# Kernel tuning notes

Measured on AMD Instinct MI355X. Metric: run time of the kernel, lower is better.

## Reference

```python
import jax, jax.numpy as jnp
import numpy as np

N_NODES = 10000
N_EDGES = 320000
N_GSO = 2
BATCH = 4
F0, F1, F2 = 64, 128, 128
K = 3


def _spmm(rows, cols, vals, x_nbf):
    """Sparse GSO multiply: (S x) for x in node-major layout [N, B, F]."""
    src = x_nbf[cols] * vals[:, None, None]            # [E, B, F]
    return jax.ops.segment_sum(src, rows, num_segments=x_nbf.shape[0])


def _graph_filter(x, edge_index, edge_vals, W, b):
    """y = sum_e sum_k S_e^k x W[e,k] + b.
    x: [B, N, Fin]; edge_index: [E_gso, 2, nnz] int; edge_vals: [E_gso, nnz];
    W: [E_gso, K, Fin, Fout]; b: [Fout]."""
    z0 = x.transpose(1, 0, 2)                          # [N, B, Fin]
    n_gso, k_taps = W.shape[0], W.shape[1]
    out = jnp.zeros((z0.shape[0], z0.shape[1], W.shape[-1]), dtype=x.dtype)
    for e in range(n_gso):
        rows, cols = edge_index[e, 0], edge_index[e, 1]
        zk = z0                                        # tap k=0 is identity
        out = out + jnp.einsum('nbf,fg->nbg', zk, W[e, 0])
        for k in range(1, k_taps):
            zk = _spmm(rows, cols, edge_vals[e], zk)   # zk = S_e zk
            out = out + jnp.einsum('nbf,fg->nbg', zk, W[e, k])
    out = out + b
    return out.transpose(1, 0, 2)                      # [B, N, Fout]


def setup_inputs() -> dict:
    key = jax.random.key(0)
    ks = jax.random.split(key, 8)
    x = jax.random.normal(ks[0], (BATCH, N_NODES, F0), dtype=jnp.float32)
    edge_index = jax.random.randint(ks[1], (N_GSO, 2, N_EDGES), 0, N_NODES, dtype=jnp.int32)
    # scale edge values ~ 1/avg_degree to keep repeated diffusion stable
    edge_vals = jax.random.uniform(ks[2], (N_GSO, N_EDGES), dtype=jnp.float32) * (1.0 / 32.0)
    W1 = jax.random.normal(ks[3], (N_GSO, K, F0, F1), dtype=jnp.float32) * 0.05
    b1 = jax.random.normal(ks[4], (F1,), dtype=jnp.float32) * 0.05
    W2 = jax.random.normal(ks[5], (N_GSO, K, F1, F2), dtype=jnp.float32) * 0.05
    b2 = jax.random.normal(ks[6], (F2,), dtype=jnp.float32) * 0.05
    return {"x": x, "edge_index": edge_index, "edge_vals": edge_vals,
            "W1": W1, "b1": b1, "W2": W2, "b2": b2}


def reference(x, edge_index, edge_vals, W1, b1, W2, b2):
    h = _graph_filter(x, edge_index, edge_vals, W1, b1)
    h = _graph_filter(h, edge_index, edge_vals, W2, b2)
    return h[:, 0, :]                                  # idxTrainMovie = 0 -> [B, F2]
```

## Files before the change

kernel.cpp:

```cpp
#include <hip/hip_runtime.h>

#define N_NODES 10000
#define N_EDGES 320000
#define BCAP    96
#define NCPY    8

__device__ __forceinline__ unsigned short f2bf(float x) {
    unsigned int u = __float_as_uint(x);
    unsigned int r = (u + 0x7fff + ((u >> 16) & 1)) >> 16;
    return (unsigned short)r;
}
__device__ __forceinline__ float bfhi(unsigned int u) { return __uint_as_float(u & 0xffff0000u); }

__global__ void bucket_kernel(const int* __restrict__ ei, const float* __restrict__ ev,
                              int* __restrict__ cnt, unsigned int* __restrict__ bkt,
                              float* __restrict__ wA) {
    int j = blockIdx.x * 256 + threadIdx.x;
    int e = j / N_EDGES, t = j - e * N_EDGES;
    int r = ei[e * 2 * N_EDGES + t];
    int c = ei[e * 2 * N_EDGES + N_EDGES + t];
    float v = ev[e * N_EDGES + t];
    int pos = atomicAdd(&cnt[e * N_NODES + c], 1);
    if (pos < BCAP)
        bkt[(e * N_NODES + c) * BCAP + pos] = ((unsigned int)f2bf(v) << 16) | (unsigned int)r;
    if (r == 0)
        atomicAdd(&wA[c * 4 + (e ? 2 : 0)], v);
}

__global__ __launch_bounds__(256) void gstage1_kernel(
        const unsigned int* __restrict__ bkt, const int* __restrict__ cnt,
        float* __restrict__ wA) {
    int t = threadIdx.x;
    int gu = (blockIdx.x << 4) + (t >> 4);
    int li = t & 15;
    int e = (gu >= N_NODES) ? 1 : 0;
    int c = gu - e * N_NODES;
    int nc = cnt[e * N_NODES + c]; if (nc > BCAP) nc = BCAP;
    const unsigned int* bp = bkt + (e * N_NODES + c) * BCAP;
    int koff = e ? 2 : 0;
    float acc = 0.f;
    for (int p = li; p < nc; p += 16) {
        unsigned int u = bp[p];
        acc += bfhi(u) * wA[(u & 0xffff) * 4 + koff];
    }
    acc += __shfl_xor(acc, 1); acc += __shfl_xor(acc, 2);
    acc += __shfl_xor(acc, 4); acc += __shfl_xor(acc, 8);
    if (li == 0) wA[c * 4 + koff + 1] = acc;
}

__global__ __launch_bounds__(256) void gstage2_kernel(
        const unsigned int* __restrict__ bkt, const int* __restrict__ cnt,
        const float* __restrict__ wA, float4* __restrict__ wB0, float4* __restrict__ wB1) {
    int t = threadIdx.x;
    int gu = (blockIdx.x << 4) + (t >> 4);
    int li = t & 15;
    int e = (gu >= N_NODES) ? 1 : 0;
    int c = gu - e * N_NODES;
    int nc = cnt[e * N_NODES + c]; if (nc > BCAP) nc = BCAP;
    const unsigned int* bp = bkt + (e * N_NODES + c) * BCAP;
    const float4* wAp = (const float4*)wA;
    float x0 = 0.f, x1 = 0.f, x2 = 0.f;
    for (int p = li; p < nc; p += 16) {
        unsigned int u = bp[p];
        float v = bfhi(u);
        float4 wr = wAp[u & 0xffff];
        if (e == 0) { x0 += wr.y * v; x1 += wr.z * v; x2 += wr.w * v; }
        else        { x0 += wr.w * v; x1 += wr.x * v; x2 += wr.y * v; }
    }
    x0 += __shfl_xor(x0, 1); x0 += __shfl_xor(x0, 2); x0 += __shfl_xor(x0, 4); x0 += __shfl_xor(x0, 8);
    x1 += __shfl_xor(x1, 1); x1 += __shfl_xor(x1, 2); x1 += __shfl_xor(x1, 4); x1 += __shfl_xor(x1, 8);
    x2 += __shfl_xor(x2, 1); x2 += __shfl_xor(x2, 2); x2 += __shfl_xor(x2, 4); x2 += __shfl_xor(x2, 8);
    if (li == 0) {
        float4 o = make_float4(x0, x1, x2, 0.f);
        if (e == 0) wB0[c] = o; else wB1[c] = o;
    }
}

__global__ __launch_bounds__(256) void gstage3_kernel(
        const unsigned int* __restrict__ bkt, const int* __restrict__ cnt,
        const float4* __restrict__ wB0, const float4* __restrict__ wB1,
        float4* __restrict__ wC0, float4* __restrict__ wC1) {
    int t = threadIdx.x;
    int gu = (blockIdx.x << 4) + (t >> 4);
    int li = t & 15;
    int e = (gu >= N_NODES) ? 1 : 0;
    int c = gu - e * N_NODES;
    int nc = cnt[e * N_NODES + c]; if (nc > BCAP) nc = BCAP;
    const unsigned int* bp = bkt + (e * N_NODES + c) * BCAP;
    const float4* win = e ? wB1 : wB0;
    float x0 = 0.f, x1 = 0.f, x2 = 0.f;
    for (int p = li; p < nc; p += 16) {
        unsigned int u = bp[p];
        float v = bfhi(u);
        float4 wr = win[u & 0xffff];
        x0 += wr.x * v; x1 += wr.y * v; x2 += wr.z * v;
    }
    x0 += __shfl_xor(x0, 1); x0 += __shfl_xor(x0, 2); x0 += __shfl_xor(x0, 4); x0 += __shfl_xor(x0, 8);
    x1 += __shfl_xor(x1, 1); x1 += __shfl_xor(x1, 2); x1 += __shfl_xor(x1, 4); x1 += __shfl_xor(x1, 8);
    x2 += __shfl_xor(x2, 1); x2 += __shfl_xor(x2, 2); x2 += __shfl_xor(x2, 4); x2 += __shfl_xor(x2, 8);
    if (li == 0) {
        float4 o = make_float4(x0, x1, x2, 0.f);
        if (e == 0) wC0[c] = o; else wC1[c] = o;
    }
}

__global__ __launch_bounds__(256) void ugemm_kernel(const float* __restrict__ x,
                                                    const float* __restrict__ wA,
                                                    const float4* __restrict__ wB0,
                                                    const float4* __restrict__ wB1,
                                                    const float4* __restrict__ wC0,
                                                    const float4* __restrict__ wC1,
                                                    float* __restrict__ U8,
                                                    float* __restrict__ S8) {
    int t = threadIdx.x;
    int b = t >> 6, f = t & 63;
    int n0 = blockIdx.x * 16;
    int cp = blockIdx.x & (NCPY - 1);
    const float* xp = x + b * (N_NODES * 64) + f;
    const float4* wAp = (const float4*)wA;
    float acc[16];
    #pragma unroll
    for (int k = 0; k < 16; ++k) acc[k] = 0.f;
    float s0 = 0.f, s1 = 0.f, s2 = 0.f, s3 = 0.f;
    #pragma unroll
    for (int j = 0; j < 16; ++j) {
        int n = n0 + j;
        float4 a  = wAp[n];
        float4 p0 = wB0[n], p1 = wB1[n];
        float4 q0 = wC0[n], q1 = wC1[n];
        float xv = xp[n * 64];
        acc[0]  += a.x * xv;  acc[1]  += a.y * xv;
        acc[2]  += a.z * xv;  acc[3]  += a.w * xv;
        acc[4]  += p0.x * xv; acc[5]  += p0.y * xv; acc[6]  += p0.z * xv;
        acc[7]  += p1.x * xv; acc[8]  += p1.y * xv; acc[9]  += p1.z * xv;
        acc[10] += q0.x * xv; acc[11] += q0.y * xv; acc[12] += q0.z * xv;
        acc[13] += q1.x * xv; acc[14] += q1.y * xv; acc[15] += q1.z * xv;
        if (t == 0) { s0 += a.x; s1 += a.y; s2 += a.z; s3 += a.w; }
    }
    float* up = U8 + cp * 4096;
    #pragma unroll
    for (int k = 0; k < 16; ++k)
        atomicAdd(&up[k * 256 + t], acc[k]);
    if (t == 0) {
        float* sp = S8 + cp * 4;
        atomicAdd(&sp[0], s0); atomicAdd(&sp[1], s1);
        atomicAdd(&sp[2], s2); atomicAdd(&sp[3], s3);
    }
}

__global__ __launch_bounds__(512) void final_T_kernel(
        const float* __restrict__ x, const float* __restrict__ U8,
        const float* __restrict__ S8,
        const float* __restrict__ W1, const float* __restrict__ b1,
        float* __restrict__ T, float* __restrict__ out) {
    __shared__ float Ws[8192];
    __shared__ float src[256];
    int blk = blockIdx.x;
    int s = blk / 5, g = blk - s * 5;
    int t = threadIdx.x;
    if (blk == 0) out[t] = 0.f;
    const int w1off[5] = { 0, 8192, 16384, 32768, 40960 };
    const float4* wsrc = (const float4*)(W1 + w1off[s]);
    const float4* wsrc0 = (const float4*)(W1 + 24576);
    float4* wdst = (float4*)Ws;
    #pragma unroll
    for (int i = 0; i < 4; ++i) {
        float4 v = wsrc[i * 512 + t];
        if (s == 0) {
            float4 v2 = wsrc0[i * 512 + t];
            v.x += v2.x; v.y += v2.y; v.z += v2.z; v.w += v2.w;
        }
        wdst[i * 512 + t] = v;
    }
    if (t < 256) {
        const int hmap[5] = { -1, 0, 1, 2, 3 };
        const int umap[4][5] = {
            { 0, 1, 4,  8, 14 },
            { 1, 4, 10, 9, 15 },
            { 2, 5, 11, 3,  7 },
            { 3, 6, 12, 7, 13 },
        };
        int k = (g == 0) ? hmap[s] : umap[g - 1][s];
        float sv;
        if (k < 0) {
            sv = x[(t >> 6) * (N_NODES * 64) + (t & 63)];
        } else {
            sv = 0.f;
            #pragma unroll
            for (int c = 0; c < NCPY; ++c) sv += U8[c * 4096 + k * 256 + t];
        }
        src[t] = sv;
    }
    __syncthreads();
    int b = t >> 7, f1 = t & 127;
    const float* sp = src + b * 64;
    float acc = 0.f;
    #pragma unroll 16
    for (int f0 = 0; f0 < 64; ++f0)
        acc += sp[f0] * Ws[f0 * 128 + f1];
    if (s == 0) {
        if (g == 0) acc += b1[f1];
        else {
            float Sg = 0.f;
            #pragma unroll
            for (int c = 0; c < NCPY; ++c) Sg += S8[c * 4 + (g - 1)];
            acc += Sg * b1[f1];
        }
    }
    atomicAdd(&T[g * 512 + t], acc);
}

__global__ __launch_bounds__(512) void final_out_kernel(
        const float* __restrict__ T, const float* __restrict__ W2,
        const float* __restrict__ b2, float* __restrict__ out) {
    __shared__ float Ws[16384];
    __shared__ float Ts[512];
    int g = blockIdx.x;
    int t = threadIdx.x;
    const int w2off[5] = { 0, 16384, 32768, 65536, 81920 };
    const float4* wsrc = (const float4*)(W2 + w2off[g]);
    const float4* wsrc0 = (const float4*)(W2 + 49152);
    float4* wdst = (float4*)Ws;
    #pragma unroll
    for (int i = 0; i < 8; ++i) {
        float4 v = wsrc[i * 512 + t];
        if (g == 0) {
            float4 v2 = wsrc0[i * 512 + t];
            v.x += v2.x; v.y += v2.y; v.z += v2.z; v.w += v2.w;
        }
        wdst[i * 512 + t] = v;
    }
    Ts[t] = T[g * 512 + t];
    __syncthreads();
    int b = t >> 7, f2 = t & 127;
    const float* tp = Ts + b * 128;
    float acc = (g == 0) ? b2[f2] : 0.f;
    #pragma unroll 16
    for (int f1 = 0; f1 < 128; ++f1)
        acc += tp[f1] * Ws[f1 * 128 + f2];
    atomicAdd(&out[t], acc);
}

extern "C" void kernel_launch(void* const* d_in, const int* in_sizes, int n_in,
                              void* d_out, int out_size, void* d_ws, size_t ws_size,
                              hipStream_t stream) {
    const float* x  = (const float*)d_in[0];
    const int*   ei = (const int*)d_in[1];
    const float* ev = (const float*)d_in[2];
    const float* W1 = (const float*)d_in[3];
    const float* b1 = (const float*)d_in[4];
    const float* W2 = (const float*)d_in[5];
    const float* b2 = (const float*)d_in[6];
    float* out = (float*)d_out;

    char* ws = (char*)d_ws;
    size_t off = 0;
    auto alloc = [&](size_t bytes) { size_t o = off; off += (bytes + 255) & ~(size_t)255; return o; };
    size_t o_bkt   = alloc((size_t)2 * N_NODES * BCAP * 4);
    size_t o_zero  = off;
    size_t o_cnt   = alloc((size_t)2 * N_NODES * 4);
    size_t o_wA    = alloc((size_t)N_NODES * 4 * 4);
    size_t o_wB0   = alloc((size_t)N_NODES * 4 * 4);
    size_t o_wB1   = alloc((size_t)N_NODES * 4 * 4);
    size_t o_wC0   = alloc((size_t)N_NODES * 4 * 4);
    size_t o_wC1   = alloc((size_t)N_NODES * 4 * 4);
    size_t o_U     = alloc((size_t)NCPY * 16 * 256 * 4);
    size_t o_S     = alloc((size_t)NCPY * 4 * 4);
    size_t o_T     = alloc((size_t)5 * 512 * 4);
    size_t zero_bytes = off - o_zero;

    unsigned int* bkt = (unsigned int*)(ws + o_bkt);
    int*    cnt   = (int*)(ws + o_cnt);
    float*  wA    = (float*)(ws + o_wA);
    float4* wB0   = (float4*)(ws + o_wB0);
    float4* wB1   = (float4*)(ws + o_wB1);
    float4* wC0   = (float4*)(ws + o_wC0);
    float4* wC1   = (float4*)(ws + o_wC1);
    float*  U8    = (float*)(ws + o_U);
    float*  S8    = (float*)(ws + o_S);
    float*  T     = (float*)(ws + o_T);

    hipMemsetAsync(ws + o_zero, 0, zero_bytes, stream);

    bucket_kernel  <<<2500, 256, 0, stream>>>(ei, ev, cnt, bkt, wA);
    gstage1_kernel <<<1250, 256, 0, stream>>>(bkt, cnt, wA);
    gstage2_kernel <<<1250, 256, 0, stream>>>(bkt, cnt, wA, wB0, wB1);
    gstage3_kernel <<<1250, 256, 0, stream>>>(bkt, cnt, wB0, wB1, wC0, wC1);
    ugemm_kernel   <<<625,  256, 0, stream>>>(x, wA, wB0, wB1, wC0, wC1, U8, S8);
    final_T_kernel <<<25,   512, 0, stream>>>(x, U8, S8, W1, b1, T, out);
    final_out_kernel<<<5,   512, 0, stream>>>(T, W2, b2, out);
}
```

Measured before the change: 163.7 us.

## Replace global-atomic edge bucketing with histogram, scan, and shared-memory fill

Edge bucketing by column used to do one global atomicAdd per edge on a counter array. It now runs in three passes. Per-chunk, per-partition histograms are built in shared memory, an exclusive scan over chunks gives each block its base offsets, and a fill pass places edges using shared-memory atomics. This removes contention on global atomics but adds two kernel launches, a histogram workspace, and reads the edge arrays eight times, once per column partition.

```diff
diff --git a/kernel.cpp b/kernel.cpp
--- a/kernel.cpp
+++ b/kernel.cpp
@@ -4,6 +4,8 @@
 #define N_EDGES 320000
 #define BCAP    96
 #define NCPY    8
+#define NCH     64
+#define HSTRIDE 1280
 
 __device__ __forceinline__ unsigned short f2bf(float x) {
     unsigned int u = __float_as_uint(x);
@@ -12,19 +14,74 @@
 }
 __device__ __forceinline__ float bfhi(unsigned int u) { return __uint_as_float(u & 0xffff0000u); }
 
-__global__ void bucket_kernel(const int* __restrict__ ei, const float* __restrict__ ev,
-                              int* __restrict__ cnt, unsigned int* __restrict__ bkt,
-                              float* __restrict__ wA) {
-    int j = blockIdx.x * 256 + threadIdx.x;
-    int e = j / N_EDGES, t = j - e * N_EDGES;
-    int r = ei[e * 2 * N_EDGES + t];
-    int c = ei[e * 2 * N_EDGES + N_EDGES + t];
-    float v = ev[e * N_EDGES + t];
-    int pos = atomicAdd(&cnt[e * N_NODES + c], 1);
-    if (pos < BCAP)
-        bkt[(e * N_NODES + c) * BCAP + pos] = ((unsigned int)f2bf(v) << 16) | (unsigned int)r;
-    if (r == 0)
-        atomicAdd(&wA[c * 4 + (e ? 2 : 0)], v);
+__global__ __launch_bounds__(256) void hist_kernel(
+        const int* __restrict__ ei, int* __restrict__ hist) {
+    __shared__ int h[1250];
+    int bid = blockIdx.x;
+    int p = bid & 7;
+    int ec = bid >> 3;
+    int e = ec / NCH, chunk = ec - e * NCH;
+    const int* cp = ei + e * 2 * N_EDGES + N_EDGES + chunk * 5000;
+    int clo = p * 1250;
+    for (int i = threadIdx.x; i < 1250; i += 256) h[i] = 0;
+    __syncthreads();
+    for (int i = threadIdx.x; i < 5000; i += 256) {
+        int c = cp[i];
+        if ((unsigned)(c - clo) < 1250u)
+            atomicAdd(&h[c - clo], 1);
+    }
+    __syncthreads();
+    int* hr = hist + bid * HSTRIDE;
+    for (int i = threadIdx.x; i < 1250; i += 256) hr[i] = h[i];
+}
+
+__global__ __launch_bounds__(256) void scan_kernel(
+        int* __restrict__ hist, int* __restrict__ cnt) {
+    int u = blockIdx.x * 256 + threadIdx.x;
+    if (u >= 2 * N_NODES) return;
+    int e = u / N_NODES;
+    int rem = u - e * N_NODES;
+    int p = rem / 1250, ci = rem - p * 1250;
+    int run = 0;
+    #pragma unroll
+    for (int k = 0; k < NCH; ++k) {
+        int* slot = hist + ((e * NCH + k) * 8 + p) * HSTRIDE + ci;
+        int v = *slot;
+        *slot = run;
+        run += v;
+    }
+    cnt[e * N_NODES + p * 1250 + ci] = run;
+}
+
+__global__ __launch_bounds__(256) void fill_kernel(
+        const int* __restrict__ ei, const float* __restrict__ ev,
+        const int* __restrict__ hist, unsigned int* __restrict__ bkt,
+        float* __restrict__ wA) {
+    __shared__ int base_l[1250];
+    int bid = blockIdx.x;
+    int p = bid & 7;
+    int ec = bid >> 3;
+    int e = ec / NCH, chunk = ec - e * NCH;
+    const int* rp = ei + e * 2 * N_EDGES + chunk * 5000;
+    const int* cp = rp + N_EDGES;
+    const float* vp = ev + e * N_EDGES + chunk * 5000;
+    int clo = p * 1250;
+    int koff = e ? 2 : 0;
+    const int* hr = hist + bid * HSTRIDE;
+    for (int i = threadIdx.x; i < 1250; i += 256) base_l[i] = hr[i];
+    __syncthreads();
+    for (int i = threadIdx.x; i < 5000; i += 256) {
+        int c = cp[i];
+        if ((unsigned)(c - clo) < 1250u) {
+            int r = rp[i];
+            float v = vp[i];
+            int pos = atomicAdd(&base_l[c - clo], 1);
+            if (pos < BCAP)
+                bkt[(e * N_NODES + c) * BCAP + pos] = ((unsigned int)f2bf(v) << 16) | (unsigned int)r;
+            if (r == 0)
+                atomicAdd(&wA[c * 4 + koff], v);
+        }
+    }
 }
 
 __global__ __launch_bounds__(256) void gstage1_kernel(
@@ -257,6 +314,7 @@
     size_t off = 0;
     auto alloc = [&](size_t bytes) { size_t o = off; off += (bytes + 255) & ~(size_t)255; return o; };
     size_t o_bkt   = alloc((size_t)2 * N_NODES * BCAP * 4);
+    size_t o_hist  = alloc((size_t)2 * NCH * 8 * HSTRIDE * 4);
     size_t o_zero  = off;
     size_t o_cnt   = alloc((size_t)2 * N_NODES * 4);
     size_t o_wA    = alloc((size_t)N_NODES * 4 * 4);
@@ -270,6 +328,7 @@
     size_t zero_bytes = off - o_zero;
 
     unsigned int* bkt = (unsigned int*)(ws + o_bkt);
+    int*    hist  = (int*)(ws + o_hist);
     int*    cnt   = (int*)(ws + o_cnt);
     float*  wA    = (float*)(ws + o_wA);
     float4* wB0   = (float4*)(ws + o_wB0);
@@ -282,7 +341,9 @@
 
     hipMemsetAsync(ws + o_zero, 0, zero_bytes, stream);
 
-    bucket_kernel  <<<2500, 256, 0, stream>>>(ei, ev, cnt, bkt, wA);
+    hist_kernel    <<<2 * NCH * 8, 256, 0, stream>>>(ei, hist);
+    scan_kernel    <<<80,   256, 0, stream>>>(hist, cnt);
+    fill_kernel    <<<2 * NCH * 8, 256, 0, stream>>>(ei, ev, hist, bkt, wA);
     gstage1_kernel <<<1250, 256, 0, stream>>>(bkt, cnt, wA);
     gstage2_kernel <<<1250, 256, 0, stream>>>(bkt, cnt, wA, wB0, wB1);
     gstage3_kernel <<<1250, 256, 0, stream>>>(bkt, cnt, wB0, wB1, wC0, wC1);
```

New measurement: 159.5 us. -2.6%, faster.

## Replace bucketed CSC gather with direct atomic edge-scatter passes

Applied to the files above, without the earlier changes.

Drops the per-column bucket construction and its bf16-packed gather stages. Each diffusion step now scans the raw COO edge list and scatter-adds into node vectors with float atomics. This avoids building the 7.7MB bucket array and removes the BCAP truncation and bf16 rounding of edge values, at the cost of one extra edge read per stage and many contended atomics (up to three per edge). The ugemm kernel is also retuned to 80 nodes per block with fewer blocks.

```diff
diff --git a/kernel.cpp b/kernel.cpp
--- a/kernel.cpp
+++ b/kernel.cpp
@@ -2,106 +2,75 @@
 
 #define N_NODES 10000
 #define N_EDGES 320000
-#define BCAP    96
 #define NCPY    8
-
-__device__ __forceinline__ unsigned short f2bf(float x) {
-    unsigned int u = __float_as_uint(x);
-    unsigned int r = (u + 0x7fff + ((u >> 16) & 1)) >> 16;
-    return (unsigned short)r;
-}
+#define UNODES  80
+#define UBLKS   125
+
 __device__ __forceinline__ float bfhi(unsigned int u) { return __uint_as_float(u & 0xffff0000u); }
 
-__global__ void bucket_kernel(const int* __restrict__ ei, const float* __restrict__ ev,
-                              int* __restrict__ cnt, unsigned int* __restrict__ bkt,
-                              float* __restrict__ wA) {
+__global__ __launch_bounds__(256) void init_kernel(
+        const int* __restrict__ ei, const float* __restrict__ ev,
+        float* __restrict__ wA) {
+    int j = blockIdx.x * 256 + threadIdx.x;
+    int e = j / N_EDGES, t = j - e * N_EDGES;
+    int r = ei[e * 2 * N_EDGES + t];
+    if (r == 0) {
+        int c = ei[e * 2 * N_EDGES + N_EDGES + t];
+        float v = ev[e * N_EDGES + t];
+        atomicAdd(&wA[c * 4 + (e ? 2 : 0)], v);
+    }
+}
+
+__global__ __launch_bounds__(256) void scat1_kernel(
+        const int* __restrict__ ei, const float* __restrict__ ev,
+        float* __restrict__ wA) {
     int j = blockIdx.x * 256 + threadIdx.x;
     int e = j / N_EDGES, t = j - e * N_EDGES;
     int r = ei[e * 2 * N_EDGES + t];
     int c = ei[e * 2 * N_EDGES + N_EDGES + t];
     float v = ev[e * N_EDGES + t];
-    int pos = atomicAdd(&cnt[e * N_NODES + c], 1);
-    if (pos < BCAP)
-        bkt[(e * N_NODES + c) * BCAP + pos] = ((unsigned int)f2bf(v) << 16) | (unsigned int)r;
-    if (r == 0)
-        atomicAdd(&wA[c * 4 + (e ? 2 : 0)], v);
-}
-
-__global__ __launch_bounds__(256) void gstage1_kernel(
-        const unsigned int* __restrict__ bkt, const int* __restrict__ cnt,
-        float* __restrict__ wA) {
-    int t = threadIdx.x;
-    int gu = (blockIdx.x << 4) + (t >> 4);
-    int li = t & 15;
-    int e = (gu >= N_NODES) ? 1 : 0;
-    int c = gu - e * N_NODES;
-    int nc = cnt[e * N_NODES + c]; if (nc > BCAP) nc = BCAP;
-    const unsigned int* bp = bkt + (e * N_NODES + c) * BCAP;
-    int koff = e ? 2 : 0;
-    float acc = 0.f;
-    for (int p = li; p < nc; p += 16) {
-        unsigned int u = bp[p];
-        acc += bfhi(u) * wA[(u & 0xffff) * 4 + koff];
-    }
-    acc += __shfl_xor(acc, 1); acc += __shfl_xor(acc, 2);
-    acc += __shfl_xor(acc, 4); acc += __shfl_xor(acc, 8);
-    if (li == 0) wA[c * 4 + koff + 1] = acc;
-}
-
-__global__ __launch_bounds__(256) void gstage2_kernel(
-        const unsigned int* __restrict__ bkt, const int* __restrict__ cnt,
-        const float* __restrict__ wA, float4* __restrict__ wB0, float4* __restrict__ wB1) {
-    int t = threadIdx.x;
-    int gu = (blockIdx.x << 4) + (t >> 4);
-    int li = t & 15;
-    int e = (gu >= N_NODES) ? 1 : 0;
-    int c = gu - e * N_NODES;
-    int nc = cnt[e * N_NODES + c]; if (nc > BCAP) nc = BCAP;
-    const unsigned int* bp = bkt + (e * N_NODES + c) * BCAP;
-    const float4* wAp = (const float4*)wA;
-    float x0 = 0.f, x1 = 0.f, x2 = 0.f;
-    for (int p = li; p < nc; p += 16) {
-        unsigned int u = bp[p];
-        float v = bfhi(u);
-        float4 wr = wAp[u & 0xffff];
-        if (e == 0) { x0 += wr.y * v; x1 += wr.z * v; x2 += wr.w * v; }
-        else        { x0 += wr.w * v; x1 += wr.x * v; x2 += wr.y * v; }
-    }
-    x0 += __shfl_xor(x0, 1); x0 += __shfl_xor(x0, 2); x0 += __shfl_xor(x0, 4); x0 += __shfl_xor(x0, 8);
-    x1 += __shfl_xor(x1, 1); x1 += __shfl_xor(x1, 2); x1 += __shfl_xor(x1, 4); x1 += __shfl_xor(x1, 8);
-    x2 += __shfl_xor(x2, 1); x2 += __shfl_xor(x2, 2); x2 += __shfl_xor(x2, 4); x2 += __shfl_xor(x2, 8);
-    if (li == 0) {
-        float4 o = make_float4(x0, x1, x2, 0.f);
-        if (e == 0) wB0[c] = o; else wB1[c] = o;
-    }
-}
-
-__global__ __launch_bounds__(256) void gstage3_kernel(
-        const unsigned int* __restrict__ bkt, const int* __restrict__ cnt,
-        const float4* __restrict__ wB0, const float4* __restrict__ wB1,
-        float4* __restrict__ wC0, float4* __restrict__ wC1) {
-    int t = threadIdx.x;
-    int gu = (blockIdx.x << 4) + (t >> 4);
-    int li = t & 15;
-    int e = (gu >= N_NODES) ? 1 : 0;
-    int c = gu - e * N_NODES;
-    int nc = cnt[e * N_NODES + c]; if (nc > BCAP) nc = BCAP;
-    const unsigned int* bp = bkt + (e * N_NODES + c) * BCAP;
-    const float4* win = e ? wB1 : wB0;
-    float x0 = 0.f, x1 = 0.f, x2 = 0.f;
-    for (int p = li; p < nc; p += 16) {
-        unsigned int u = bp[p];
-        float v = bfhi(u);
-        float4 wr = win[u & 0xffff];
-        x0 += wr.x * v; x1 += wr.y * v; x2 += wr.z * v;
-    }
-    x0 += __shfl_xor(x0, 1); x0 += __shfl_xor(x0, 2); x0 += __shfl_xor(x0, 4); x0 += __shfl_xor(x0, 8);
-    x1 += __shfl_xor(x1, 1); x1 += __shfl_xor(x1, 2); x1 += __shfl_xor(x1, 4); x1 += __shfl_xor(x1, 8);
-    x2 += __shfl_xor(x2, 1); x2 += __shfl_xor(x2, 2); x2 += __shfl_xor(x2, 4); x2 += __shfl_xor(x2, 8);
-    if (li == 0) {
-        float4 o = make_float4(x0, x1, x2, 0.f);
-        if (e == 0) wC0[c] = o; else wC1[c] = o;
-    }
+    if (e == 0) atomicAdd(&wA[c * 4 + 1], wA[r * 4 + 0] * v);
+    else        atomicAdd(&wA[c * 4 + 3], wA[r * 4 + 2] * v);
+}
+
+__global__ __launch_bounds__(256) void scat2_kernel(
+        const int* __restrict__ ei, const float* __restrict__ ev,
+        const float* __restrict__ wA,
+        float* __restrict__ wB0, float* __restrict__ wB1) {
+    int j = blockIdx.x * 256 + threadIdx.x;
+    int e = j / N_EDGES, t = j - e * N_EDGES;
+    int r = ei[e * 2 * N_EDGES + t];
+    int c = ei[e * 2 * N_EDGES + N_EDGES + t];
+    float v = ev[e * N_EDGES + t];
+    float4 wr = ((const float4*)wA)[r];
+    if (e == 0) {
+        float* dst = wB0 + c * 4;
+        atomicAdd(dst + 0, wr.y * v);
+        atomicAdd(dst + 1, wr.z * v);
+        atomicAdd(dst + 2, wr.w * v);
+    } else {
+        float* dst = wB1 + c * 4;
+        atomicAdd(dst + 0, wr.w * v);
+        atomicAdd(dst + 1, wr.x * v);
+        atomicAdd(dst + 2, wr.y * v);
+    }
+}
+
+__global__ __launch_bounds__(256) void scat3_kernel(
+        const int* __restrict__ ei, const float* __restrict__ ev,
+        const float* __restrict__ wB0, const float* __restrict__ wB1,
+        float* __restrict__ wC0, float* __restrict__ wC1) {
+    int j = blockIdx.x * 256 + threadIdx.x;
+    int e = j / N_EDGES, t = j - e * N_EDGES;
+    int r = ei[e * 2 * N_EDGES + t];
+    int c = ei[e * 2 * N_EDGES + N_EDGES + t];
+    float v = ev[e * N_EDGES + t];
+    const float4* win = (const float4*)(e ? wB1 : wB0);
+    float* dst = (e ? wC1 : wC0) + c * 4;
+    float4 wr = win[r];
+    atomicAdd(dst + 0, wr.x * v);
+    atomicAdd(dst + 1, wr.y * v);
+    atomicAdd(dst + 2, wr.z * v);
 }
 
 __global__ __launch_bounds__(256) void ugemm_kernel(const float* __restrict__ x,
@@ -114,7 +83,7 @@
                                                     float* __restrict__ S8) {
     int t = threadIdx.x;
     int b = t >> 6, f = t & 63;
-    int n0 = blockIdx.x * 16;
+    int n0 = blockIdx.x * UNODES;
     int cp = blockIdx.x & (NCPY - 1);
     const float* xp = x + b * (N_NODES * 64) + f;
     const float4* wAp = (const float4*)wA;
@@ -122,8 +91,8 @@
     #pragma unroll
     for (int k = 0; k < 16; ++k) acc[k] = 0.f;
     float s0 = 0.f, s1 = 0.f, s2 = 0.f, s3 = 0.f;
-    #pragma unroll
-    for (int j = 0; j < 16; ++j) {
+    #pragma unroll 8
+    for (int j = 0; j < UNODES; ++j) {
         int n = n0 + j;
         float4 a  = wAp[n];
         float4 p0 = wB0[n], p1 = wB1[n];
@@ -256,9 +225,7 @@
     char* ws = (char*)d_ws;
     size_t off = 0;
     auto alloc = [&](size_t bytes) { size_t o = off; off += (bytes + 255) & ~(size_t)255; return o; };
-    size_t o_bkt   = alloc((size_t)2 * N_NODES * BCAP * 4);
     size_t o_zero  = off;
-    size_t o_cnt   = alloc((size_t)2 * N_NODES * 4);
     size_t o_wA    = alloc((size_t)N_NODES * 4 * 4);
     size_t o_wB0   = alloc((size_t)N_NODES * 4 * 4);
     size_t o_wB1   = alloc((size_t)N_NODES * 4 * 4);
@@ -269,24 +236,23 @@
     size_t o_T     = alloc((size_t)5 * 512 * 4);
     size_t zero_bytes = off - o_zero;
 
-    unsigned int* bkt = (unsigned int*)(ws + o_bkt);
-    int*    cnt   = (int*)(ws + o_cnt);
     float*  wA    = (float*)(ws + o_wA);
-    float4* wB0   = (float4*)(ws + o_wB0);
-    float4* wB1   = (float4*)(ws + o_wB1);
-    float4* wC0   = (float4*)(ws + o_wC0);
-    float4* wC1   = (float4*)(ws + o_wC1);
+    float*  wB0   = (float*)(ws + o_wB0);
+    float*  wB1   = (float*)(ws + o_wB1);
+    float*  wC0   = (float*)(ws + o_wC0);
+    float*  wC1   = (float*)(ws + o_wC1);
     float*  U8    = (float*)(ws + o_U);
     float*  S8    = (float*)(ws + o_S);
     float*  T     = (float*)(ws + o_T);
 
     hipMemsetAsync(ws + o_zero, 0, zero_bytes, stream);
 
-    bucket_kernel  <<<2500, 256, 0, stream>>>(ei, ev, cnt, bkt, wA);
-    gstage1_kernel <<<1250, 256, 0, stream>>>(bkt, cnt, wA);
-    gstage2_kernel <<<1250, 256, 0, stream>>>(bkt, cnt, wA, wB0, wB1);
-    gstage3_kernel <<<1250, 256, 0, stream>>>(bkt, cnt, wB0, wB1, wC0, wC1);
-    ugemm_kernel   <<<625,  256, 0, stream>>>(x, wA, wB0, wB1, wC0, wC1, U8, S8);
+    init_kernel  <<<2500, 256, 0, stream>>>(ei, ev, wA);
+    scat1_kernel <<<2500, 256, 0, stream>>>(ei, ev, wA);
+    scat2_kernel <<<2500, 256, 0, stream>>>(ei, ev, wA, wB0, wB1);
+    scat3_kernel <<<2500, 256, 0, stream>>>(ei, ev, wB0, wB1, wC0, wC1);
+    ugemm_kernel <<<UBLKS, 256, 0, stream>>>(x, wA, (const float4*)wB0, (const float4*)wB1,
+                                             (const float4*)wC0, (const float4*)wC1, U8, S8);
     final_T_kernel <<<25,   512, 0, stream>>>(x, U8, S8, W1, b1, T, out);
     final_out_kernel<<<5,   512, 0, stream>>>(T, W2, b2, out);
 }
```

Result: slower. 395.3 us (+141.5%).
